# Performance work log

Measured on AMD Instinct MI355X. Metric: run time of the kernel, lower is better.

Reference implementation:

```python
import jax, jax.numpy as jnp
import numpy as np

S = 7
COORD = 5.0
NOOBJ = 0.5

def _mse_sum(a, b):
    # nn.MSELoss(reduction='sum') with broadcasting, as in the source
    return jnp.sum((a - b) ** 2)

def _calc_iou(reg_pred, nb):
    # reg_pred: [10,7,7] = [conf0,x0,y0,w0,h0,conf1,x1,y1,w1,h1]; nb: [4] gt box / 448
    # NB: source treats gt as corner-format (x1 = nb[0]) and pred as center-format.
    def one(box):  # box: [4,7,7]
        x1 = jnp.maximum(nb[0], box[0] - box[2] * 0.5)
        y1 = jnp.maximum(nb[1], box[1] - box[3] * 0.5)
        w = jnp.minimum(nb[0] + nb[2], box[0] + box[2] * 0.5) - x1
        h = jnp.minimum(nb[1] + nb[3], box[1] + box[3] * 0.5) - y1
        inter = jnp.clip(w, 0.0) * jnp.clip(h, 0.0)
        area = box[2] * box[3]
        return inter / (area + nb[2] * nb[3] - inter + 1e-6)
    return jnp.stack([one(reg_pred[1:5]), one(reg_pred[6:10])], axis=0)  # [2,7,7]

def _image_loss(pred_b, annot_b):
    # pred_b: [30,7,7] (post-sigmoid), annot_b: [n_boxes,5] pixel coords (x,y,w,h,cls)
    cls_pred = pred_b[:20]
    reg_pred = pred_b[20:]

    def step(carry, bbox):
        cls_target, gt_boxes, loss = carry  # state accumulates across boxes, as in source
        label = bbox[4].astype(jnp.int32)
        cls_target = cls_target.at[label].set(1.0)
        px = jnp.floor((bbox[0] + bbox[2] * 0.5) * S / 448.0).astype(jnp.int32)
        py = jnp.floor((bbox[1] + bbox[3] * 0.5) * S / 448.0).astype(jnp.int32)
        gt_boxes = gt_boxes.at[px, py].set(1.0)
        nb = bbox[:4] / 448.0
        iou = _calc_iou(reg_pred, nb)  # [2,7,7]
        best = jnp.argmax(iou, axis=0).astype(pred_b.dtype)  # [7,7], 1 -> box1 responsible
        xy0 = COORD * gt_boxes * best * (_mse_sum(nb[0], reg_pred[6]) + _mse_sum(nb[1], reg_pred[7]))
        xy1 = COORD * gt_boxes * (1.0 - best) * (_mse_sum(nb[0], reg_pred[1]) + _mse_sum(nb[1], reg_pred[2]))
        wh0 = COORD * gt_boxes * best * (_mse_sum(jnp.sqrt(nb[2]), jnp.sqrt(reg_pred[8])) + _mse_sum(jnp.sqrt(nb[3]), jnp.sqrt(reg_pred[9])))
        wh1 = COORD * gt_boxes * (1.0 - best) * (_mse_sum(jnp.sqrt(nb[2]), jnp.sqrt(reg_pred[3])) + _mse_sum(jnp.sqrt(nb[3]), jnp.sqrt(reg_pred[4])))
        conf0 = gt_boxes * iou[0] * best * _mse_sum(1.0, reg_pred[0])
        conf1 = gt_boxes * iou[1] * (1.0 - best) * _mse_sum(1.0, reg_pred[5])
        nconf0 = NOOBJ * (1.0 - gt_boxes) * iou[0] * best * _mse_sum(0.0, reg_pred[0])
        nconf1 = NOOBJ * (1.0 - gt_boxes) * iou[1] * (1.0 - best) * _mse_sum(0.0, reg_pred[5])
        cls_l = gt_boxes * _mse_sum(cls_target, cls_pred)
        loss = loss + jnp.sum(xy0 + xy1 + wh0 + wh1 + conf0 + conf1 + nconf0 + nconf1 + cls_l)
        return (cls_target, gt_boxes, loss), None

    init = (jnp.zeros((20, S, S), pred_b.dtype),
            jnp.zeros((S, S), pred_b.dtype),
            jnp.zeros((), pred_b.dtype))
    (_, _, loss), _ = jax.lax.scan(step, init, annot_b)
    return loss

def setup_inputs():
    key = jax.random.key(0)
    k1, k2, k3, k4, k5 = jax.random.split(key, 5)
    B, NBOX = 128, 8
    pred = jax.random.normal(k1, (B, 30, S, S), dtype=jnp.float32)
    img = jax.random.normal(k2, (B, 3, 448, 448), dtype=jnp.float32)
    # Valid (non-padded) boxes: x,y in [0,300), w,h in [10,140) so grid idx stays in [0,7)
    xy = jax.random.uniform(k3, (B, NBOX, 2), dtype=jnp.float32) * 300.0
    wh = jax.random.uniform(k4, (B, NBOX, 2), dtype=jnp.float32) * 130.0 + 10.0
    cls = jax.random.randint(k5, (B, NBOX, 1), 0, 20).astype(jnp.float32)
    annot = jnp.concatenate([xy, wh, cls], axis=-1)  # [B,NBOX,5]
    return {"pred": pred, "img": img, "annot": annot}

def reference(pred, img, annot):
    predictions = jax.nn.sigmoid(pred)  # [B,30,7,7]
    # img is threaded through but unused by the loss math (as in the source)
    per_image = jax.vmap(_image_loss)(predictions, annot)  # [B]
    return jnp.sum(per_image).reshape(1)
```

## Files before the change

### kernel.cpp

```cpp
#include <hip/hip_runtime.h>
#include <math.h>


#define GRID_S 7
#define NCELL 49
#define NBOX 8

__device__ __forceinline__ float sigmoidf_(float x) {
    return 1.0f / (1.0f + expf(-x));
}

__device__ __forceinline__ float wave_sum(float v) {
#pragma unroll
    for (int off = 32; off > 0; off >>= 1)
        v += __shfl_xor(v, off, 64);
    return v;
}

__global__ __launch_bounds__(64) void yolo_loss_kernel(
    const float* __restrict__ pred,
    const float* __restrict__ annot,
    float* __restrict__ out)
{
    const int b = blockIdx.x;
    const int k = threadIdx.x;
    const float active = (k < NCELL) ? 1.0f : 0.0f;
    const int kc = (k < NCELL) ? k : (NCELL - 1);

    const float* pb = pred + (size_t)b * 30 * NCELL;
    const float* ab = annot + (size_t)b * NBOX * 5;

    float an[NBOX * 5];
#pragma unroll
    for (int i = 0; i < NBOX * 5; ++i) an[i] = ab[i];

    float r[10];
#pragma unroll
    for (int c = 0; c < 10; ++c)
        r[c] = sigmoidf_(pb[(20 + c) * NCELL + kc]);
    const float sr3 = sqrtf(r[3]), sr4 = sqrtf(r[4]);
    const float sr8 = sqrtf(r[8]), sr9 = sqrtf(r[9]);

    const float Sconf1 = wave_sum((1.0f - r[0]) * (1.0f - r[0]) * active);
    const float Sconf5 = wave_sum((1.0f - r[5]) * (1.0f - r[5]) * active);
    const float Sn0    = wave_sum(r[0] * r[0] * active);
    const float Sn5    = wave_sum(r[5] * r[5] * active);

    float p2 = 0.0f;
#pragma unroll
    for (int c = 0; c < 20; ++c) {
        float v = sigmoidf_(pb[c * NCELL + kc]);
        p2 += v * v * active;
    }
    const float Ptot = wave_sum(p2);

    float gt = 0.0f;
    unsigned seen = 0u;
    float clsdelta = 0.0f;
    float local = 0.0f;

#pragma unroll
    for (int t = 0; t < NBOX; ++t) {
        const float b0 = an[t * 5 + 0], b1 = an[t * 5 + 1];
        const float b2 = an[t * 5 + 2], b3 = an[t * 5 + 3];
        const float b4 = an[t * 5 + 4];

        int lbl = (int)b4;
        lbl = lbl < 0 ? 0 : (lbl > 19 ? 19 : lbl);
        if (!((seen >> lbl) & 1u)) {
            seen |= (1u << lbl);
            float v = sigmoidf_(pb[lbl * NCELL + kc]);
            float Sl = wave_sum(v * active);
            clsdelta += 49.0f - 2.0f * Sl;
        }

        int px = (int)floorf((b0 + b2 * 0.5f) * 7.0f / 448.0f);
        int py = (int)floorf((b1 + b3 * 0.5f) * 7.0f / 448.0f);
        px = px < 0 ? 0 : (px > 6 ? 6 : px);
        py = py < 0 ? 0 : (py > 6 ? 6 : py);
        const int cell = px * GRID_S + py;
        if (k == cell) gt = 1.0f;

        const float nb0 = b0 / 448.0f, nb1 = b1 / 448.0f;
        const float nb2 = b2 / 448.0f, nb3 = b3 / 448.0f;
        const float snb2 = sqrtf(nb2), snb3 = sqrtf(nb3);

        const float A = wave_sum(((nb0 - r[6]) * (nb0 - r[6]) +
                                  (nb1 - r[7]) * (nb1 - r[7])) * active);
        const float B = wave_sum(((nb0 - r[1]) * (nb0 - r[1]) +
                                  (nb1 - r[2]) * (nb1 - r[2])) * active);
        const float C = wave_sum(((snb2 - sr8) * (snb2 - sr8) +
                                  (snb3 - sr9) * (snb3 - sr9)) * active);
        const float D = wave_sum(((snb2 - sr3) * (snb2 - sr3) +
                                  (snb3 - sr4) * (snb3 - sr4)) * active);

        float iou0, iou1;
        {
            const float cx = r[1], cy = r[2], w = r[3], h = r[4];
            const float x1 = fmaxf(nb0, cx - w * 0.5f);
            const float y1 = fmaxf(nb1, cy - h * 0.5f);
            const float ww = fminf(nb0 + nb2, cx + w * 0.5f) - x1;
            const float hh = fminf(nb1 + nb3, cy + h * 0.5f) - y1;
            const float inter = fmaxf(ww, 0.0f) * fmaxf(hh, 0.0f);
            iou0 = inter / (w * h + nb2 * nb3 - inter + 1e-6f);
        }
        {
            const float cx = r[6], cy = r[7], w = r[8], h = r[9];
            const float x1 = fmaxf(nb0, cx - w * 0.5f);
            const float y1 = fmaxf(nb1, cy - h * 0.5f);
            const float ww = fminf(nb0 + nb2, cx + w * 0.5f) - x1;
            const float hh = fminf(nb1 + nb3, cy + h * 0.5f) - y1;
            const float inter = fmaxf(ww, 0.0f) * fmaxf(hh, 0.0f);
            iou1 = inter / (w * h + nb2 * nb3 - inter + 1e-6f);
        }
        const float best = (iou1 > iou0) ? 1.0f : 0.0f;

        const float cls_scalar = Ptot + clsdelta;
        const float contrib =
            gt * (best * 5.0f * (A + C) + (1.0f - best) * 5.0f * (B + D)
                  + best * iou0 * Sconf1 + (1.0f - best) * iou1 * Sconf5
                  + cls_scalar)
            + (1.0f - gt) * 0.5f * (best * iou0 * Sn0 + (1.0f - best) * iou1 * Sn5);

        local += contrib * active;
    }

    const float tot = wave_sum(local);
    if (k == 0) atomicAdd(out, tot);
}

extern "C" void kernel_launch(void* const* d_in, const int* in_sizes, int n_in,
                              void* d_out, int out_size, void* d_ws, size_t ws_size,
                              hipStream_t stream) {
    const float* pred  = (const float*)d_in[0];
    const float* annot = (const float*)d_in[2];
    float* out = (float*)d_out;

    (void)in_sizes; (void)n_in; (void)d_ws; (void)ws_size; (void)out_size;

    yolo_loss_kernel<<<128, 64, 0, stream>>>(pred, annot, out);
}
```

Measured before the change: 344.9 us.

## Expand squared-error sums into precomputed moments and batch all wave reductions

```diff
diff --git a/kernel.cpp b/kernel.cpp
--- a/kernel.cpp
+++ b/kernel.cpp
@@ -5,16 +5,10 @@
 #define GRID_S 7
 #define NCELL 49
 #define NBOX 8
+#define NSUM 41
 
 __device__ __forceinline__ float sigmoidf_(float x) {
     return 1.0f / (1.0f + expf(-x));
-}
-
-__device__ __forceinline__ float wave_sum(float v) {
-#pragma unroll
-    for (int off = 32; off > 0; off >>= 1)
-        v += __shfl_xor(v, off, 64);
-    return v;
 }
 
 __global__ __launch_bounds__(64) void yolo_loss_kernel(
@@ -41,18 +35,46 @@
     const float sr3 = sqrtf(r[3]), sr4 = sqrtf(r[4]);
     const float sr8 = sqrtf(r[8]), sr9 = sqrtf(r[9]);
 
-    const float Sconf1 = wave_sum((1.0f - r[0]) * (1.0f - r[0]) * active);
-    const float Sconf5 = wave_sum((1.0f - r[5]) * (1.0f - r[5]) * active);
-    const float Sn0    = wave_sum(r[0] * r[0] * active);
-    const float Sn5    = wave_sum(r[5] * r[5] * active);
-
+    float s[NSUM];
     float p2 = 0.0f;
 #pragma unroll
     for (int c = 0; c < 20; ++c) {
         float v = sigmoidf_(pb[c * NCELL + kc]);
-        p2 += v * v * active;
+        s[c] = v * active;
+        p2 += v * v;
     }
-    const float Ptot = wave_sum(p2);
+    s[20] = p2 * active;
+    s[21] = r[1] * active;
+    s[22] = r[2] * active;
+    s[23] = r[1] * r[1] * active;
+    s[24] = r[2] * r[2] * active;
+    s[25] = r[6] * active;
+    s[26] = r[7] * active;
+    s[27] = r[6] * r[6] * active;
+    s[28] = r[7] * r[7] * active;
+    s[29] = sr3 * active;
+    s[30] = sr4 * active;
+    s[31] = sr8 * active;
+    s[32] = sr9 * active;
+    s[33] = r[3] * active;
+    s[34] = r[4] * active;
+    s[35] = r[8] * active;
+    s[36] = r[9] * active;
+    s[37] = (1.0f - r[0]) * (1.0f - r[0]) * active;
+    s[38] = (1.0f - r[5]) * (1.0f - r[5]) * active;
+    s[39] = r[0] * r[0] * active;
+    s[40] = r[5] * r[5] * active;
+
+#pragma unroll
+    for (int off = 32; off > 0; off >>= 1) {
+#pragma unroll
+        for (int i = 0; i < NSUM; ++i)
+            s[i] += __shfl_xor(s[i], off, 64);
+    }
+
+    const float Ptot   = s[20];
+    const float Sconf1 = s[37], Sconf5 = s[38];
+    const float Sn0    = s[39], Sn5    = s[40];
 
     float gt = 0.0f;
     unsigned seen = 0u;
@@ -69,8 +91,9 @@
         lbl = lbl < 0 ? 0 : (lbl > 19 ? 19 : lbl);
         if (!((seen >> lbl) & 1u)) {
             seen |= (1u << lbl);
-            float v = sigmoidf_(pb[lbl * NCELL + kc]);
-            float Sl = wave_sum(v * active);
+            float Sl = 0.0f;
+#pragma unroll
+            for (int c = 0; c < 20; ++c) Sl += (c == lbl) ? s[c] : 0.0f;
             clsdelta += 49.0f - 2.0f * Sl;
         }
 
@@ -85,14 +108,12 @@
         const float nb2 = b2 / 448.0f, nb3 = b3 / 448.0f;
         const float snb2 = sqrtf(nb2), snb3 = sqrtf(nb3);
 
-        const float A = wave_sum(((nb0 - r[6]) * (nb0 - r[6]) +
-                                  (nb1 - r[7]) * (nb1 - r[7])) * active);
-        const float B = wave_sum(((nb0 - r[1]) * (nb0 - r[1]) +
-                                  (nb1 - r[2]) * (nb1 - r[2])) * active);
-        const float C = wave_sum(((snb2 - sr8) * (snb2 - sr8) +
-                                  (snb3 - sr9) * (snb3 - sr9)) * active);
-        const float D = wave_sum(((snb2 - sr3) * (snb2 - sr3) +
-                                  (snb3 - sr4) * (snb3 - sr4)) * active);
+        const float nxy = nb0 * nb0 + nb1 * nb1;
+        const float nwh = nb2 + nb3;
+        const float A = 49.0f * nxy - 2.0f * (nb0 * s[25] + nb1 * s[26]) + (s[27] + s[28]);
+        const float B = 49.0f * nxy - 2.0f * (nb0 * s[21] + nb1 * s[22]) + (s[23] + s[24]);
+        const float C = 49.0f * nwh - 2.0f * (snb2 * s[31] + snb3 * s[32]) + (s[35] + s[36]);
+        const float D = 49.0f * nwh - 2.0f * (snb2 * s[29] + snb3 * s[30]) + (s[33] + s[34]);
 
         float iou0, iou1;
         {
@@ -125,7 +146,10 @@
         local += contrib * active;
     }
 
-    const float tot = wave_sum(local);
+    float tot = local;
+#pragma unroll
+    for (int off = 32; off > 0; off >>= 1)
+        tot += __shfl_xor(tot, off, 64);
     if (k == 0) atomicAdd(out, tot);
 }
 
```

Result: no change. 344.7 us (-0.1%).
